# Optimization experiments

Measured on AMD Instinct MI355X. Metric: run time of the kernel, lower is better.

## Reference

```python
import jax, jax.numpy as jnp
import numpy as np

C_M, C_Z, C_H = 256, 128, 32
EPS = 1e-3
LN_EPS = 1e-5


def setup_inputs() -> dict:
    key = jax.random.key(0)
    ks = jax.random.split(key, 8)
    B, S, N = 1, 128, 256
    m = jax.random.normal(ks[0], (B, S, N, C_M), dtype=jnp.float32)
    msa_mask = jnp.ones((B, S, N), dtype=jnp.float32)
    sa = 1.0 / np.sqrt(C_M)
    so = 1.0 / np.sqrt(C_H * C_H)
    return {
        "m": m,
        "msa_mask": msa_mask,
        "ln_g": jnp.ones((C_M,), jnp.float32),
        "ln_b": jnp.zeros((C_M,), jnp.float32),
        "Wa": jax.random.normal(ks[1], (C_M, C_H), jnp.float32) * sa,
        "ba": jax.random.normal(ks[2], (C_H,), jnp.float32) * 0.01,
        "Wb": jax.random.normal(ks[3], (C_M, C_H), jnp.float32) * sa,
        "bb": jax.random.normal(ks[4], (C_H,), jnp.float32) * 0.01,
        "Wo": jax.random.normal(ks[5], (C_H * C_H, C_Z), jnp.float32) * so,
        "bo": jax.random.normal(ks[6], (C_Z,), jnp.float32) * 0.01,
    }


def reference(m, msa_mask, ln_g, ln_b, Wa, ba, Wb, bb, Wo, bo):
    # m: [B, S, N, c_m], msa_mask: [B, S, N]
    mask = msa_mask[..., None]                       # [B, S, N, 1]
    mu = jnp.mean(m, axis=-1, keepdims=True)
    var = jnp.mean(jnp.square(m - mu), axis=-1, keepdims=True)
    mn = (m - mu) * jax.lax.rsqrt(var + LN_EPS) * ln_g + ln_b
    a = (mn @ Wa + ba) * mask                        # [B, S, N, c_h]
    b = (mn @ Wb + bb) * mask                        # [B, S, N, c_h]
    # outer product, summed over the MSA sequence axis s
    outer = jnp.einsum('bsic,bsje->bijce', a, b)     # [B, N, N, c_h, c_h]
    Bsz, N = m.shape[0], m.shape[2]
    outer = outer.reshape(Bsz, N, N, C_H * C_H)
    out = outer @ Wo + bo                            # [B, N, N, c_z]
    norm = jnp.einsum('bsi,bsj->bij', msa_mask, msa_mask)[..., None] + EPS
    return out / norm
```

## Files before the change

kernel.cpp:

```cpp
#include <hip/hip_runtime.h>

typedef unsigned short u16;
typedef short bf16x8 __attribute__((ext_vector_type(8)));
typedef float f32x4 __attribute__((ext_vector_type(4)));

#define CM 256

__device__ inline u16 f2bf(float f) {
    union { float f; unsigned u; } v; v.f = f;
    unsigned r = v.u + 0x7fffu + ((v.u >> 16) & 1u);
    return (u16)(r >> 16);
}

__global__ void kW(const float* __restrict__ Wo, const float* __restrict__ Wa,
                   const float* __restrict__ Wb, u16* __restrict__ Wo_t,
                   u16* __restrict__ Wab_t)
{
    int bid = blockIdx.x, t = threadIdx.x;
    if (bid < 512) {
        int idx = bid * 256 + t;
        int ce = idx >> 7, z = idx & 127;
        int c = ce >> 5, e = ce & 31;
        Wo_t[z * 1024 + e * 32 + c] = f2bf(Wo[idx]);
    } else {
        int idx = (bid - 512) * 256 + t;
        int n = idx >> 8, k = idx & 255;
        float v = (n < 32) ? Wa[k * 32 + n] : Wb[k * 32 + (n - 32)];
        Wab_t[idx] = f2bf(v);
    }
}

__global__ void kN(const float* __restrict__ mask, float* __restrict__ norm_ws)
{
    int i = blockIdx.x, j = threadIdx.x;
    float acc = 1e-3f;
    for (int s = 0; s < 128; s++)
        acc += mask[s * 256 + i] * mask[s * 256 + j];
    norm_ws[i * 256 + j] = acc;
}

__global__ __launch_bounds__(256, 2) void kA(
    const float* __restrict__ m, const float* __restrict__ mask,
    const float* __restrict__ ln_g, const float* __restrict__ ln_b,
    const u16* __restrict__ Wab_t, const float* __restrict__ ba,
    const float* __restrict__ bb,
    u16* __restrict__ a_t, u16* __restrict__ b_t)
{
    __shared__ u16 mn_s[64 * 264];

    const int t = threadIdx.x;
    const int w = t >> 6, lane = t & 63, quad = lane >> 4, lr = lane & 15;
    const int r0 = blockIdx.x * 64;

    bf16x8 wf[8];
    for (int ks = 0; ks < 8; ks++)
        wf[ks] = *(const bf16x8*)(Wab_t + (w * 16 + lr) * 256 + ks * 32 + quad * 8);

    const float4 g4  = ((const float4*)ln_g)[lane];
    const float4 be4 = ((const float4*)ln_b)[lane];

    for (int rr = 0; rr < 16; rr++) {
        int r = w * 16 + rr;
        float4 x = ((const float4*)m)[(r0 + r) * 64 + lane];
        float s1 = x.x + x.y + x.z + x.w;
        float s2 = x.x * x.x + x.y * x.y + x.z * x.z + x.w * x.w;
        for (int off = 32; off; off >>= 1) {
            s1 += __shfl_xor(s1, off);
            s2 += __shfl_xor(s2, off);
        }
        float mu = s1 * (1.f / CM);
        float rstd = rsqrtf(s2 * (1.f / CM) - mu * mu + 1e-5f);
        ushort4 o;
        o.x = f2bf((x.x - mu) * rstd * g4.x + be4.x);
        o.y = f2bf((x.y - mu) * rstd * g4.y + be4.y);
        o.z = f2bf((x.z - mu) * rstd * g4.z + be4.z);
        o.w = f2bf((x.w - mu) * rstd * g4.w + be4.w);
        *(ushort4*)(&mn_s[r * 264 + lane * 4]) = o;
    }
    __syncthreads();

    f32x4 acc[4] = {};
    for (int ks = 0; ks < 8; ks++)
        for (int mt = 0; mt < 4; mt++) {
            bf16x8 af = *(const bf16x8*)(&mn_s[(mt * 16 + lr) * 264 + ks * 32 + quad * 8]);
            acc[mt] = __builtin_amdgcn_mfma_f32_16x16x32_bf16(af, wf[ks], acc[mt], 0, 0, 0);
        }

    const int n = w * 16 + lr;
    const int cc = n & 31;
    const bool isB = n >= 32;
    const float bv = isB ? bb[cc] : ba[cc];
    u16* dst = isB ? b_t : a_t;
    for (int mt = 0; mt < 4; mt++)
        for (int reg = 0; reg < 4; reg++) {
            int r = mt * 16 + quad * 4 + reg;
            int row = r0 + r;
            int s = row >> 8, i = row & 255;
            float val = (acc[mt][reg] + bv) * mask[row];
            dst[(i * 32 + cc) * 128 + s] = f2bf(val);
        }
}

__global__ __launch_bounds__(256, 2) void kB(
    const u16* __restrict__ a_t, const u16* __restrict__ b_t,
    const u16* __restrict__ Wo_t, const float* __restrict__ bo,
    const float* __restrict__ norm_ws, float* __restrict__ out)
{
    __shared__ __align__(16) u16 smem[32768];
    u16* a_s = smem;
    u16* b_s = smem + 128 * 72;
    u16* outer_s = smem;

    const int t = threadIdx.x;
    const int w = t >> 6, lane = t & 63, quad = lane >> 4, lr = lane & 15;
    const int wm = w >> 1, wn = w & 1;
    const u16* ag = a_t + blockIdx.x * (128 * 128);
    const u16* bg = b_t + blockIdx.y * (256 * 128);

    f32x4 acc2[4][8] = {};
    for (int kh = 0; kh < 2; kh++) {
        for (int q = 0; q < 4; q++) {
            int flat = q * 2048 + t * 8;
            int mm = flat >> 6, kk = flat & 63;
            *(uint4*)(&a_s[mm * 72 + kk]) = *(const uint4*)(ag + mm * 128 + kh * 64 + kk);
        }
        for (int q = 0; q < 8; q++) {
            int flat = q * 2048 + t * 8;
            int mm = flat >> 6, kk = flat & 63;
            *(uint4*)(&b_s[mm * 72 + kk]) = *(const uint4*)(bg + mm * 128 + kh * 64 + kk);
        }
        __syncthreads();
        for (int ks = 0; ks < 2; ks++) {
            int k0 = ks * 32 + quad * 8;
            bf16x8 af[4], bfr[8];
            for (int tm = 0; tm < 4; tm++)
                af[tm] = *(const bf16x8*)(&a_s[(wm * 64 + tm * 16 + lr) * 72 + k0]);
            for (int tn = 0; tn < 8; tn++)
                bfr[tn] = *(const bf16x8*)(&b_s[(wn * 128 + tn * 16 + lr) * 72 + k0]);
            for (int tm = 0; tm < 4; tm++)
                for (int tn = 0; tn < 8; tn++)
                    acc2[tm][tn] = __builtin_amdgcn_mfma_f32_16x16x32_bf16(
                        af[tm], bfr[tn], acc2[tm][tn], 0, 0, 0);
        }
        __syncthreads();
    }

    for (int tm = 0; tm < 4; tm++) {
        int mbase = wm * 64 + tm * 16 + quad * 4;
        int i_l = mbase >> 5, cb = mbase & 31;
        for (int tn = 0; tn < 8; tn++) {
            int n_loc = wn * 128 + tn * 16 + lr;
            int j_l = n_loc >> 5, e = n_loc & 31;
            int p = i_l * 8 + j_l;
            int cI = e * 4 + (cb >> 3);
            int f = (cI * 5 + p) & 127;
            ushort4 o;
            o.x = f2bf(acc2[tm][tn][0]);
            o.y = f2bf(acc2[tm][tn][1]);
            o.z = f2bf(acc2[tm][tn][2]);
            o.w = f2bf(acc2[tm][tn][3]);
            *(ushort4*)(&outer_s[p * 1024 + f * 8 + (cb & 7)]) = o;
        }
    }
    __syncthreads();

    const int n0w = w * 32;
    const u16* wp0 = Wo_t + (n0w + lr) * 1024;
    const u16* wp1 = Wo_t + (n0w + 16 + lr) * 1024;
    f32x4 acc3[2][2] = {};
    bf16x8 b3c[2], b3n[2];
    {
        int k0 = quad * 8;
        b3c[0] = *(const bf16x8*)(wp0 + k0);
        b3c[1] = *(const bf16x8*)(wp1 + k0);
        b3n[0] = *(const bf16x8*)(wp0 + 32 + k0);
        b3n[1] = *(const bf16x8*)(wp1 + 32 + k0);
    }
    for (int ks = 0; ks < 32; ks++) {
        int cI = ks * 4 + quad;
        bf16x8 a3[2];
        for (int mt = 0; mt < 2; mt++) {
            int p = mt * 16 + lr;
            int f = (cI * 5 + p) & 127;
            a3[mt] = *(const bf16x8*)(&outer_s[p * 1024 + f * 8]);
        }
        bf16x8 pf0, pf1;
        if (ks < 30) {
            int k2 = (ks + 2) * 32 + quad * 8;
            pf0 = *(const bf16x8*)(wp0 + k2);
            pf1 = *(const bf16x8*)(wp1 + k2);
        }
        for (int mt = 0; mt < 2; mt++) {
            acc3[mt][0] = __builtin_amdgcn_mfma_f32_16x16x32_bf16(a3[mt], b3c[0], acc3[mt][0], 0, 0, 0);
            acc3[mt][1] = __builtin_amdgcn_mfma_f32_16x16x32_bf16(a3[mt], b3c[1], acc3[mt][1], 0, 0, 0);
        }
        b3c[0] = b3n[0]; b3c[1] = b3n[1];
        b3n[0] = pf0;    b3n[1] = pf1;
    }

    const int i0 = blockIdx.x * 4, j0 = blockIdx.y * 8;
    for (int mt = 0; mt < 2; mt++)
        for (int reg = 0; reg < 4; reg++) {
            int p = mt * 16 + quad * 4 + reg;
            int ii = i0 + (p >> 3), jj = j0 + (p & 7);
            float nrm = norm_ws[ii * 256 + jj];
            for (int tt = 0; tt < 2; tt++) {
                int z = n0w + tt * 16 + lr;
                out[(ii * 256 + jj) * 128 + z] = (acc3[mt][tt][reg] + bo[z]) / nrm;
            }
        }
}

extern "C" void kernel_launch(void* const* d_in, const int* in_sizes, int n_in,
                              void* d_out, int out_size, void* d_ws, size_t ws_size,
                              hipStream_t stream)
{
    const float* m    = (const float*)d_in[0];
    const float* mask = (const float*)d_in[1];
    const float* ln_g = (const float*)d_in[2];
    const float* ln_b = (const float*)d_in[3];
    const float* Wa   = (const float*)d_in[4];
    const float* ba   = (const float*)d_in[5];
    const float* Wb   = (const float*)d_in[6];
    const float* bb   = (const float*)d_in[7];
    const float* Wo   = (const float*)d_in[8];
    const float* bo   = (const float*)d_in[9];
    float* out = (float*)d_out;

    char* ws = (char*)d_ws;
    u16*   a_t     = (u16*)ws;
    u16*   b_t     = (u16*)(ws + 0x200000);
    u16*   Wo_t    = (u16*)(ws + 0x400000);
    u16*   Wab_t   = (u16*)(ws + 0x440000);
    float* norm_ws = (float*)(ws + 0x448000);

    hipLaunchKernelGGL(kW, dim3(576), dim3(256), 0, stream, Wo, Wa, Wb, Wo_t, Wab_t);
    hipLaunchKernelGGL(kN, dim3(256), dim3(256), 0, stream, mask, norm_ws);
    hipLaunchKernelGGL(kA, dim3(512), dim3(256), 0, stream,
                       m, mask, ln_g, ln_b, Wab_t, ba, bb, a_t, b_t);
    hipLaunchKernelGGL(kB, dim3(64, 32), dim3(256), 0, stream,
                       a_t, b_t, Wo_t, bo, norm_ws, out);
}
```

Measured before the change: 199.7 us.

## Load MFMA operands directly from global, permute Wo layout, merge norm kernel

Folds the mask-norm kernel into the weight-prep kernel, saving one launch. In kB the first GEMM now reads A/B fragments straight from global memory instead of staging them through LDS with barriers. The outer-product tile is written to LDS with an XOR swizzle. Wo's K dimension is permuted to match the new accumulator-to-K ordering, so the second GEMM can read the tile contiguously. The trade-off is more redundant global/L2 traffic for operand loads across waves, in exchange for removing the LDS staging and its syncs.

```diff
diff --git a/kernel.cpp b/kernel.cpp
--- a/kernel.cpp
+++ b/kernel.cpp
@@ -12,31 +12,33 @@
     return (u16)(r >> 16);
 }
 
+
 __global__ void kW(const float* __restrict__ Wo, const float* __restrict__ Wa,
-                   const float* __restrict__ Wb, u16* __restrict__ Wo_t,
-                   u16* __restrict__ Wab_t)
+                   const float* __restrict__ Wb, const float* __restrict__ mask,
+                   u16* __restrict__ Wo_t, u16* __restrict__ Wab_t,
+                   float* __restrict__ norm_ws)
 {
     int bid = blockIdx.x, t = threadIdx.x;
     if (bid < 512) {
         int idx = bid * 256 + t;
         int ce = idx >> 7, z = idx & 127;
         int c = ce >> 5, e = ce & 31;
-        Wo_t[z * 1024 + e * 32 + c] = f2bf(Wo[idx]);
-    } else {
+        int kpp = (c & 3) | ((e & 1) << 2) | (((c >> 2) & 1) << 3)
+                | (((e >> 1) & 7) << 4) | (((c >> 3) & 1) << 7)
+                | ((e >> 4) << 8) | ((c >> 4) << 9);
+        Wo_t[z * 1024 + kpp] = f2bf(Wo[idx]);
+    } else if (bid < 576) {
         int idx = (bid - 512) * 256 + t;
         int n = idx >> 8, k = idx & 255;
         float v = (n < 32) ? Wa[k * 32 + n] : Wb[k * 32 + (n - 32)];
         Wab_t[idx] = f2bf(v);
-    }
-}
-
-__global__ void kN(const float* __restrict__ mask, float* __restrict__ norm_ws)
-{
-    int i = blockIdx.x, j = threadIdx.x;
-    float acc = 1e-3f;
-    for (int s = 0; s < 128; s++)
-        acc += mask[s * 256 + i] * mask[s * 256 + j];
-    norm_ws[i * 256 + j] = acc;
+    } else {
+        int i = bid - 576, j = t;
+        float acc = 1e-3f;
+        for (int s = 0; s < 128; s++)
+            acc += mask[s * 256 + i] * mask[s * 256 + j];
+        norm_ws[i * 256 + j] = acc;
+    }
 }
 
 __global__ __launch_bounds__(256, 2) void kA(
@@ -106,10 +108,7 @@
     const u16* __restrict__ Wo_t, const float* __restrict__ bo,
     const float* __restrict__ norm_ws, float* __restrict__ out)
 {
-    __shared__ __align__(16) u16 smem[32768];
-    u16* a_s = smem;
-    u16* b_s = smem + 128 * 72;
-    u16* outer_s = smem;
+    __shared__ __align__(16) u16 outer_s[32 * 1024];
 
     const int t = threadIdx.x;
     const int w = t >> 6, lane = t & 63, quad = lane >> 4, lr = lane & 15;
@@ -118,50 +117,32 @@
     const u16* bg = b_t + blockIdx.y * (256 * 128);
 
     f32x4 acc2[4][8] = {};
-    for (int kh = 0; kh < 2; kh++) {
-        for (int q = 0; q < 4; q++) {
-            int flat = q * 2048 + t * 8;
-            int mm = flat >> 6, kk = flat & 63;
-            *(uint4*)(&a_s[mm * 72 + kk]) = *(const uint4*)(ag + mm * 128 + kh * 64 + kk);
-        }
-        for (int q = 0; q < 8; q++) {
-            int flat = q * 2048 + t * 8;
-            int mm = flat >> 6, kk = flat & 63;
-            *(uint4*)(&b_s[mm * 72 + kk]) = *(const uint4*)(bg + mm * 128 + kh * 64 + kk);
-        }
-        __syncthreads();
-        for (int ks = 0; ks < 2; ks++) {
-            int k0 = ks * 32 + quad * 8;
-            bf16x8 af[4], bfr[8];
-            for (int tm = 0; tm < 4; tm++)
-                af[tm] = *(const bf16x8*)(&a_s[(wm * 64 + tm * 16 + lr) * 72 + k0]);
+    for (int ks = 0; ks < 4; ks++) {
+        const int k0 = ks * 32 + quad * 8;
+        bf16x8 af[4], bfr[8];
+        for (int tm = 0; tm < 4; tm++)
+            af[tm] = *(const bf16x8*)(ag + (wm * 64 + tm * 16 + lr) * 128 + k0);
+        for (int tn = 0; tn < 8; tn++)
+            bfr[tn] = *(const bf16x8*)(bg + (wn * 128 + tn * 16 + lr) * 128 + k0);
+        for (int tm = 0; tm < 4; tm++)
             for (int tn = 0; tn < 8; tn++)
-                bfr[tn] = *(const bf16x8*)(&b_s[(wn * 128 + tn * 16 + lr) * 72 + k0]);
-            for (int tm = 0; tm < 4; tm++)
-                for (int tn = 0; tn < 8; tn++)
-                    acc2[tm][tn] = __builtin_amdgcn_mfma_f32_16x16x32_bf16(
-                        af[tm], bfr[tn], acc2[tm][tn], 0, 0, 0);
-        }
-        __syncthreads();
-    }
-
-    for (int tm = 0; tm < 4; tm++) {
-        int mbase = wm * 64 + tm * 16 + quad * 4;
-        int i_l = mbase >> 5, cb = mbase & 31;
+                acc2[tm][tn] = __builtin_amdgcn_mfma_f32_16x16x32_bf16(
+                    af[tm], bfr[tn], acc2[tm][tn], 0, 0, 0);
+    }
+
+    for (int tm = 0; tm < 4; tm++)
         for (int tn = 0; tn < 8; tn++) {
-            int n_loc = wn * 128 + tn * 16 + lr;
-            int j_l = n_loc >> 5, e = n_loc & 31;
-            int p = i_l * 8 + j_l;
-            int cI = e * 4 + (cb >> 3);
-            int f = (cI * 5 + p) & 127;
+            int p  = (wm * 2 + (tm >> 1)) * 8 + wn * 4 + (tn >> 1);
+            int cI = (quad & 1) | ((lr >> 1) << 1) | ((quad >> 1) << 4)
+                   | ((tn & 1) << 5) | ((tm & 1) << 6);
+            int pi = cI ^ (p & 7);
             ushort4 o;
             o.x = f2bf(acc2[tm][tn][0]);
             o.y = f2bf(acc2[tm][tn][1]);
             o.z = f2bf(acc2[tm][tn][2]);
             o.w = f2bf(acc2[tm][tn][3]);
-            *(ushort4*)(&outer_s[p * 1024 + f * 8 + (cb & 7)]) = o;
-        }
-    }
+            *(ushort4*)(&outer_s[p * 1024 + pi * 8 + 4 * (lr & 1)]) = o;
+        }
     __syncthreads();
 
     const int n0w = w * 32;
@@ -177,12 +158,10 @@
         b3n[1] = *(const bf16x8*)(wp1 + 32 + k0);
     }
     for (int ks = 0; ks < 32; ks++) {
-        int cI = ks * 4 + quad;
         bf16x8 a3[2];
         for (int mt = 0; mt < 2; mt++) {
-            int p = mt * 16 + lr;
-            int f = (cI * 5 + p) & 127;
-            a3[mt] = *(const bf16x8*)(&outer_s[p * 1024 + f * 8]);
+            int pi = ((ks * 4 + quad) ^ (lr & 7));
+            a3[mt] = *(const bf16x8*)(&outer_s[(mt * 16 + lr) * 1024 + pi * 8]);
         }
         bf16x8 pf0, pf1;
         if (ks < 30) {
@@ -234,8 +213,8 @@
     u16*   Wab_t   = (u16*)(ws + 0x440000);
     float* norm_ws = (float*)(ws + 0x448000);
 
-    hipLaunchKernelGGL(kW, dim3(576), dim3(256), 0, stream, Wo, Wa, Wb, Wo_t, Wab_t);
-    hipLaunchKernelGGL(kN, dim3(256), dim3(256), 0, stream, mask, norm_ws);
+    hipLaunchKernelGGL(kW, dim3(832), dim3(256), 0, stream,
+                       Wo, Wa, Wb, mask, Wo_t, Wab_t, norm_ws);
     hipLaunchKernelGGL(kA, dim3(512), dim3(256), 0, stream,
                        m, mask, ln_g, ln_b, Wab_t, ba, bb, a_t, b_t);
     hipLaunchKernelGGL(kB, dim3(64, 32), dim3(256), 0, stream,
```

Result: slower. 231.9 us (+16.1%).
